# Kernel tuning notes

Measured on AMD Instinct MI355X. Metric: run time of the kernel, lower is better.

Reference implementation:

```python
import jax, jax.numpy as jnp
import numpy as np

DIM = 128
HEADS = 4
DIM_HEAD = 32
N_EMBD = HEADS * DIM_HEAD  # 128
SCALE = DIM_HEAD ** -0.5


def conv2d(x, w, b):
    # NCHW conv, 3x3, stride 1, SAME padding (= padding=1 in torch)
    out = jax.lax.conv_general_dilated(
        x, w, window_strides=(1, 1), padding='SAME',
        dimension_numbers=('NCHW', 'OIHW', 'NCHW'))
    return out + b[None, :, None, None]


def conv_block(x, w1, b1, w2, b2):
    # Conv -> ReLU -> Conv (the to_q/to_k/to_v pattern)
    return conv2d(jax.nn.relu(conv2d(x, w1, b1)), w2, b2)


def setup_inputs() -> dict:
    key = jax.random.key(0)
    ks = jax.random.split(key, 20)
    B, C, S = 4, DIM, 32
    H, W = 128, 512
    wscale = 0.05

    def cw(k, cout, cin):
        return jax.random.normal(k, (cout, cin, 3, 3), jnp.float32) * wscale

    inp = {
        'x': jax.random.normal(ks[0], (B, C, S, S), jnp.float32),
        'y': jax.random.normal(ks[1], (B, C, H, W), jnp.float32),
        'u': jax.random.randint(ks[2], (B, S, S), 0, W),
        'q_w1': cw(ks[3], N_EMBD, DIM), 'q_b1': jnp.zeros((N_EMBD,), jnp.float32),
        'q_w2': cw(ks[4], N_EMBD, N_EMBD), 'q_b2': jnp.zeros((N_EMBD,), jnp.float32),
        'k_w1': cw(ks[5], N_EMBD, DIM), 'k_b1': jnp.zeros((N_EMBD,), jnp.float32),
        'k_w2': cw(ks[6], N_EMBD, N_EMBD), 'k_b2': jnp.zeros((N_EMBD,), jnp.float32),
        'v_w1': cw(ks[7], N_EMBD, DIM), 'v_b1': jnp.zeros((N_EMBD,), jnp.float32),
        'v_w2': cw(ks[8], N_EMBD, N_EMBD), 'v_b2': jnp.zeros((N_EMBD,), jnp.float32),
        'proj_w': cw(ks[9], DIM, N_EMBD), 'proj_b': jnp.zeros((DIM,), jnp.float32),
    }
    return inp


def reference(x, y, u, q_w1, q_b1, q_w2, q_b2, k_w1, k_b1, k_w2, k_b2,
              v_w1, v_b1, v_w2, v_b2, proj_w, proj_b):
    B, C, S, _ = x.shape
    _, _, H, W = y.shape
    SS = S * S

    # Q from the (B,C,S,S) query grid -> (B, S^2, n_embd)
    q = conv_block(x, q_w1, q_b1, q_w2, q_b2).reshape(B, N_EMBD, SS).transpose(0, 2, 1)

    # K, V from the (B,C,H,W) map
    k = conv_block(y, k_w1, k_b1, k_w2, k_b2)  # (B, E, H, W)
    v = conv_block(y, v_w1, v_b1, v_w2, v_b2)

    # Gather columns of K/V along W per query index u (clamped)
    uc = jnp.clip(u, 0, W - 1).astype(jnp.int32).reshape(B, 1, 1, SS)
    ks = jnp.take_along_axis(k, uc, axis=3).transpose(0, 3, 2, 1)  # (B, SS, H, E)
    vs = jnp.take_along_axis(v, uc, axis=3).transpose(0, 3, 2, 1)  # (B, SS, H, E)

    # Per-query attention over the H axis
    dot = SCALE * jnp.einsum('bqe,bqhe->bqh', q, ks)  # (B, SS, H)
    attn = jax.nn.softmax(dot, axis=-1)
    a = jnp.einsum('bqh,bqhe->bqe', attn, vs)  # (B, SS, E)

    a = a.transpose(0, 2, 1).reshape(B, N_EMBD, S, S)
    z = jax.nn.relu(conv2d(a, proj_w, proj_b))  # (B, DIM, S, S)
    return z
```

## Files before the change

### kernel.cpp

```cpp
#include <hip/hip_runtime.h>
#include <stdint.h>

typedef __attribute__((ext_vector_type(16))) float f32x16;
typedef __attribute__((ext_vector_type(8))) short s16x8;

__device__ inline short bf16b(float f) {
  uint32_t x = __float_as_uint(f);
  return (short)((x + 0x7fffu + ((x >> 16) & 1u)) >> 16);
}
__device__ inline float bfu(uint16_t u) { return __uint_as_float(((uint32_t)u) << 16); }

__device__ inline void gll16(const void* g, void* l) {
  __builtin_amdgcn_global_load_lds((const __attribute__((address_space(1))) void*)g,
                                   (__attribute__((address_space(3))) void*)l, 16, 0, 0);
}

__global__ __launch_bounds__(256) void packw_k(
    const float* w0, const float* w1, const float* w2, const float* w3,
    const float* w4, const float* w5, const float* w6, s16x8* dst) {
  const float* srcs[7] = {w0, w1, w2, w3, w4, w5, w6};
  const int widx = blockIdx.y;
  const float* src = srcs[widx];
  const int gid = blockIdx.x * 256 + threadIdx.x;
  const int lane = gid & 63, frag = gid >> 6;
  const int nblk = frag & 3, ks = (frag >> 2) & 1, chunk = (frag >> 3) & 3, tap = frag >> 5;
  const int co = nblk * 32 + (lane & 31);
  const int cib = chunk * 32 + ks * 16 + (lane >> 5) * 8;
  s16x8 v;
#pragma unroll
  for (int j = 0; j < 8; ++j)
    v[j] = bf16b(src[((size_t)co * 128 + cib + j) * 9 + tap]);
  dst[(size_t)widx * 18432 + (size_t)frag * 64 + lane] = v;
}

template <int TW>
__global__ __launch_bounds__(256) void nchw2nhwc_k(
    const float* __restrict__ in, uint16_t* __restrict__ out, int H, int W) {
  __shared__ float tile[128][TW + 1];
  const int b = blockIdx.z, h = blockIdx.y, w0 = blockIdx.x * TW;
  for (int idx = threadIdx.x; idx < 128 * TW; idx += 256) {
    int c = idx / TW, w = idx - c * TW;
    tile[c][w] = in[(((size_t)b * 128 + c) * H + h) * W + w0 + w];
  }
  __syncthreads();
  for (int idx = threadIdx.x; idx < TW * 16; idx += 256) {
    int w = idx >> 4, cg = idx & 15;
    s16x8 v;
#pragma unroll
    for (int j = 0; j < 8; ++j) v[j] = bf16b(tile[cg * 8 + j][w]);
    *reinterpret_cast<s16x8*>(out + ((((size_t)b * H + h) * W + w0 + w) << 7) + cg * 8) = v;
  }
}

template <int OMODE, bool RELU, typename Tout>
__global__ __launch_bounds__(256, 3) void convmf4_k(
    const uint16_t* __restrict__ in, const s16x8* __restrict__ wpk,
    const float* __restrict__ bias, Tout* __restrict__ out,
    const uint16_t* __restrict__ zp, int H, int W) {
  constexpr int CP = 34, RP = 6, RPCP = RP * CP;
  constexpr int SLOTS = 4 * RPCP;
  constexpr int SPT = 4;
  __shared__ s16x8 lds[2][SPT * 256];
  const int b = blockIdx.z, r0 = blockIdx.y * 4, c0 = blockIdx.x * 32;
  const int tid = threadIdx.x, lane = tid & 63, wn = tid >> 6;
  const int wbase = tid & 192;

  const uint16_t* gsrc[SPT];
#pragma unroll
  for (int i = 0; i < SPT; ++i) {
    const int s = tid + i * 256;
    const int kq = s / RPCP;
    const int rem = s - kq * RPCP;
    const int r = rem / CP, c = rem - r * CP;
    const int gr = r0 + r - 1, gc = c0 + c - 1;
    const bool ok = (s < SLOTS) && gr >= 0 && gr < H && gc >= 0 && gc < W;
    gsrc[i] = ok ? (in + (((size_t)b * H + gr) * W + gc) * 128 + kq * 8) : zp;
  }

  const s16x8* __restrict__ wbl = wpk + wn * 64 + lane;
  s16x8 wf[9];
#pragma unroll
  for (int t = 0; t < 9; ++t) wf[t] = wbl[t * 2048];

#pragma unroll
  for (int i = 0; i < SPT; ++i) gll16(gsrc[i], &lds[0][wbase + i * 256]);

  f32x16 acc[4];
#pragma unroll
  for (int i = 0; i < 4; ++i)
#pragma unroll
    for (int r = 0; r < 16; ++r) acc[i][r] = 0.f;

  const int abase = (lane >> 5) * RPCP + (lane & 31);
  __syncthreads();

#pragma unroll
  for (int chunk = 0; chunk < 4; ++chunk) {
    const int cb = chunk & 1;
    if (chunk < 3) {
#pragma unroll
      for (int i = 0; i < SPT; ++i)
        gll16(gsrc[i] + (chunk + 1) * 32, &lds[cb ^ 1][wbase + i * 256]);
    }
    const s16x8* __restrict__ Lb = &lds[cb][abase];
#pragma unroll
    for (int ks = 0; ks < 2; ++ks) {
#pragma unroll
      for (int kx = 0; kx < 3; ++kx) {
        s16x8 ar[6];
#pragma unroll
        for (int r = 0; r < 6; ++r) ar[r] = Lb[ks * 2 * RPCP + r * CP + kx];
        __builtin_amdgcn_s_setprio(1);
#pragma unroll
        for (int ky = 0; ky < 3; ++ky) {
#pragma unroll
          for (int mf = 0; mf < 4; ++mf)
            acc[mf] = __builtin_amdgcn_mfma_f32_32x32x16_bf16(ar[mf + ky], wf[ky * 3 + kx],
                                                              acc[mf], 0, 0, 0);
        }
        __builtin_amdgcn_s_setprio(0);
        if (!(chunk == 3 && ks == 1)) {
          const int nc = (ks == 0) ? chunk : chunk + 1;
          const int nks = (ks == 0) ? 1 : 0;
#pragma unroll
          for (int ky = 0; ky < 3; ++ky) {
            const int tap = ky * 3 + kx;
            wf[tap] = wbl[((tap * 4 + nc) * 2 + nks) * 256];
          }
        }
      }
    }
    if (chunk < 3) __syncthreads();
  }

  const int co = wn * 32 + (lane & 31);
  const float bv = bias[co];
#pragma unroll
  for (int mf = 0; mf < 4; ++mf) {
    const int gr = r0 + mf;
#pragma unroll
    for (int reg = 0; reg < 16; ++reg) {
      const int gc = c0 + (reg & 3) + 8 * (reg >> 2) + 4 * (lane >> 5);
      float v = acc[mf][reg] + bv;
      if (RELU) v = fmaxf(v, 0.f);
      size_t idx;
      if (OMODE == 0)      idx = (((size_t)b * H + gr) * W + gc) * 128 + co;
      else if (OMODE == 1) idx = (((size_t)b * W + gc) * H + gr) * 128 + co;
      else                 idx = (((size_t)b * 128 + co) * H + gr) * W + gc;
      if constexpr (sizeof(Tout) == 2) ((uint16_t*)out)[idx] = (uint16_t)bf16b(v);
      else out[idx] = v;
    }
  }
}

__global__ __launch_bounds__(128) void attn_dot_k(
    const float* __restrict__ qg, const uint16_t* __restrict__ Kg,
    const int* __restrict__ u, float* __restrict__ pout) {
  const int bs = blockIdx.x;
  const int b = bs >> 10;
  const int tid = threadIdx.x;
  __shared__ float sq[128], sd[128];
  sq[tid] = qg[(size_t)bs * 128 + tid];
  int w = u[bs]; w = w < 0 ? 0 : (w > 511 ? 511 : w);
  __syncthreads();
  const uint32_t* kp = reinterpret_cast<const uint32_t*>(
      Kg + (((size_t)b * 512 + w) * 128 + tid) * 128);
  float acc = 0.f;
#pragma unroll 8
  for (int i = 0; i < 64; ++i) {
    uint32_t v = kp[i];
    acc = fmaf(sq[2 * i],     __uint_as_float(v << 16), acc);
    acc = fmaf(sq[2 * i + 1], __uint_as_float(v & 0xffff0000u), acc);
  }
  sd[tid] = acc * 0.17677669529663687f;
  __syncthreads();
  float mx = -1e30f;
  for (int i = 0; i < 128; ++i) mx = fmaxf(mx, sd[i]);
  float e = expf(sd[tid] - mx);
  __syncthreads();
  sd[tid] = e;
  __syncthreads();
  float sum = 0.f;
  for (int i = 0; i < 128; ++i) sum += sd[i];
  pout[(size_t)bs * 128 + tid] = e / sum;
}

__global__ __launch_bounds__(128) void attn_pv_k(
    const float* __restrict__ pin, const uint16_t* __restrict__ Vg,
    const int* __restrict__ u, uint16_t* __restrict__ aout) {
  const int bs = blockIdx.x;
  const int b = bs >> 10;
  const int tid = threadIdx.x;
  __shared__ float sp[128];
  sp[tid] = pin[(size_t)bs * 128 + tid];
  int w = u[bs]; w = w < 0 ? 0 : (w > 511 ? 511 : w);
  __syncthreads();
  const uint16_t* vp = Vg + ((size_t)b * 512 + w) * 16384 + tid;
  float acc = 0.f;
#pragma unroll 8
  for (int h = 0; h < 128; ++h)
    acc = fmaf(sp[h], bfu(vp[h * 128]), acc);
  aout[(size_t)bs * 128 + tid] = (uint16_t)bf16b(acc);
}

extern "C" void kernel_launch(void* const* d_in, const int* in_sizes, int n_in,
                              void* d_out, int out_size, void* d_ws, size_t ws_size,
                              hipStream_t stream) {
  const float* x      = (const float*)d_in[0];
  const float* y      = (const float*)d_in[1];
  const int*   u      = (const int*)d_in[2];
  const float* q_w1   = (const float*)d_in[3];
  const float* q_b1   = (const float*)d_in[4];
  const float* q_w2   = (const float*)d_in[5];
  const float* q_b2   = (const float*)d_in[6];
  const float* k_w1   = (const float*)d_in[7];
  const float* k_b1   = (const float*)d_in[8];
  const float* k_w2   = (const float*)d_in[9];
  const float* k_b2   = (const float*)d_in[10];
  const float* v_w1   = (const float*)d_in[11];
  const float* v_b1   = (const float*)d_in[12];
  const float* v_w2   = (const float*)d_in[13];
  const float* v_b2   = (const float*)d_in[14];
  const float* proj_w = (const float*)d_in[15];
  const float* proj_b = (const float*)d_in[16];
  float* out = (float*)d_out;

  char* ws = (char*)d_ws;
  const size_t MB = 1 << 20;
  const size_t BIG = 64 * MB;
  const bool tierB = ws_size >= 203 * MB;
  uint16_t* A  = (uint16_t*)ws;
  uint16_t* Bb = (uint16_t*)(ws + BIG);
  uint16_t* KV = tierB ? (uint16_t*)(ws + 2 * BIG) : A;
  char* sm = ws + (tierB ? 3 : 2) * BIG;
  float*    qg  = (float*)sm;
  float*    pb  = (float*)(sm + 2 * MB);
  uint16_t* xbf = (uint16_t*)(sm + 4 * MB);
  uint16_t* t1  = (uint16_t*)(sm + 5 * MB);
  uint16_t* ab  = (uint16_t*)(sm + 6 * MB);
  s16x8*    wpk = (s16x8*)(sm + 7 * MB);
  uint16_t* zp  = (uint16_t*)(sm + 10 * MB);

  hipMemsetAsync(zp, 0, 1024, stream);
  packw_k<<<dim3(72, 7), 256, 0, stream>>>(q_w1, q_w2, k_w1, k_w2, v_w1, v_w2, proj_w, wpk);
  nchw2nhwc_k<32><<<dim3(1, 32, 4), 256, 0, stream>>>(x, xbf, 32, 32);
  nchw2nhwc_k<64><<<dim3(8, 128, 4), 256, 0, stream>>>(y, A, 128, 512);
  convmf4_k<0, true,  uint16_t><<<dim3(1, 8, 4), 256, 0, stream>>>(xbf, wpk + 0 * 18432, q_b1, t1, zp, 32, 32);
  convmf4_k<0, false, float   ><<<dim3(1, 8, 4), 256, 0, stream>>>(t1,  wpk + 1 * 18432, q_b2, qg, zp, 32, 32);
  convmf4_k<0, true,  uint16_t><<<dim3(16, 32, 4), 256, 0, stream>>>(A,  wpk + 2 * 18432, k_b1, Bb, zp, 128, 512);
  convmf4_k<1, false, uint16_t><<<dim3(16, 32, 4), 256, 0, stream>>>(Bb, wpk + 3 * 18432, k_b2, KV, zp, 128, 512);
  attn_dot_k<<<dim3(4096), 128, 0, stream>>>(qg, KV, u, pb);
  if (!tierB) nchw2nhwc_k<64><<<dim3(8, 128, 4), 256, 0, stream>>>(y, A, 128, 512);
  convmf4_k<0, true,  uint16_t><<<dim3(16, 32, 4), 256, 0, stream>>>(A,  wpk + 4 * 18432, v_b1, Bb, zp, 128, 512);
  convmf4_k<1, false, uint16_t><<<dim3(16, 32, 4), 256, 0, stream>>>(Bb, wpk + 5 * 18432, v_b2, KV, zp, 128, 512);
  attn_pv_k<<<dim3(4096), 128, 0, stream>>>(pb, KV, u, ab);
  convmf4_k<3, true, float><<<dim3(1, 8, 4), 256, 0, stream>>>(ab, wpk + 6 * 18432, proj_b, out, zp, 32, 32);
}
```

Measured before the change: 438.0 us.

## Triple-buffer conv input tiles with explicit vmcnt waits and raw barriers

Changes the implicit-GEMM conv kernel from double to triple buffering of LDS input chunks. Two chunks are prefetched up front, and each later prefetch is issued after compute, so global loads run two chunks ahead. Full __syncthreads are replaced with s_waitcnt vmcnt counts plus raw s_barrier, so only the needed loads are waited on. This costs more LDS per block, which may reduce occupancy, and the hand-tuned vmcnt counts depend on how many weight loads are still outstanding.

New measurement: 433.4 us. Within noise of the previous version (-1.0%).

```diff
diff --git a/kernel.cpp b/kernel.cpp
--- a/kernel.cpp
+++ b/kernel.cpp
@@ -3,6 +3,8 @@
 
 typedef __attribute__((ext_vector_type(16))) float f32x16;
 typedef __attribute__((ext_vector_type(8))) short s16x8;
+
+#define WAITVM(n) asm volatile("s_waitcnt vmcnt(" #n ")" ::: "memory")
 
 __device__ inline short bf16b(float f) {
   uint32_t x = __float_as_uint(f);
@@ -53,14 +55,14 @@
 }
 
 template <int OMODE, bool RELU, typename Tout>
-__global__ __launch_bounds__(256, 3) void convmf4_k(
+__global__ __launch_bounds__(256, 3) void convmf5_k(
     const uint16_t* __restrict__ in, const s16x8* __restrict__ wpk,
     const float* __restrict__ bias, Tout* __restrict__ out,
     const uint16_t* __restrict__ zp, int H, int W) {
   constexpr int CP = 34, RP = 6, RPCP = RP * CP;
   constexpr int SLOTS = 4 * RPCP;
   constexpr int SPT = 4;
-  __shared__ s16x8 lds[2][SPT * 256];
+  __shared__ s16x8 lds[3][SPT * 256];
   const int b = blockIdx.z, r0 = blockIdx.y * 4, c0 = blockIdx.x * 32;
   const int tid = threadIdx.x, lane = tid & 63, wn = tid >> 6;
   const int wbase = tid & 192;
@@ -84,6 +86,8 @@
 
 #pragma unroll
   for (int i = 0; i < SPT; ++i) gll16(gsrc[i], &lds[0][wbase + i * 256]);
+#pragma unroll
+  for (int i = 0; i < SPT; ++i) gll16(gsrc[i] + 32, &lds[1][wbase + i * 256]);
 
   f32x16 acc[4];
 #pragma unroll
@@ -92,17 +96,13 @@
     for (int r = 0; r < 16; ++r) acc[i][r] = 0.f;
 
   const int abase = (lane >> 5) * RPCP + (lane & 31);
-  __syncthreads();
+  WAITVM(6);
+  __builtin_amdgcn_s_barrier();
+  __builtin_amdgcn_sched_barrier(0);
 
 #pragma unroll
   for (int chunk = 0; chunk < 4; ++chunk) {
-    const int cb = chunk & 1;
-    if (chunk < 3) {
-#pragma unroll
-      for (int i = 0; i < SPT; ++i)
-        gll16(gsrc[i] + (chunk + 1) * 32, &lds[cb ^ 1][wbase + i * 256]);
-    }
-    const s16x8* __restrict__ Lb = &lds[cb][abase];
+    const s16x8* __restrict__ Lb = &lds[chunk % 3][abase];
 #pragma unroll
     for (int ks = 0; ks < 2; ++ks) {
 #pragma unroll
@@ -130,7 +130,21 @@
         }
       }
     }
-    if (chunk < 3) __syncthreads();
+    __builtin_amdgcn_sched_barrier(0);
+    if (chunk < 2) {
+#pragma unroll
+      for (int i = 0; i < SPT; ++i)
+        gll16(gsrc[i] + (chunk + 2) * 32, &lds[(chunk + 2) % 3][wbase + i * 256]);
+    }
+    if (chunk == 0 || chunk == 1) {
+      WAITVM(24);
+      __builtin_amdgcn_s_barrier();
+      __builtin_amdgcn_sched_barrier(0);
+    } else if (chunk == 2) {
+      WAITVM(18);
+      __builtin_amdgcn_s_barrier();
+      __builtin_amdgcn_sched_barrier(0);
+    }
   }
 
   const int co = wn * 32 + (lane & 31);
@@ -245,14 +259,14 @@
   packw_k<<<dim3(72, 7), 256, 0, stream>>>(q_w1, q_w2, k_w1, k_w2, v_w1, v_w2, proj_w, wpk);
   nchw2nhwc_k<32><<<dim3(1, 32, 4), 256, 0, stream>>>(x, xbf, 32, 32);
   nchw2nhwc_k<64><<<dim3(8, 128, 4), 256, 0, stream>>>(y, A, 128, 512);
-  convmf4_k<0, true,  uint16_t><<<dim3(1, 8, 4), 256, 0, stream>>>(xbf, wpk + 0 * 18432, q_b1, t1, zp, 32, 32);
-  convmf4_k<0, false, float   ><<<dim3(1, 8, 4), 256, 0, stream>>>(t1,  wpk + 1 * 18432, q_b2, qg, zp, 32, 32);
-  convmf4_k<0, true,  uint16_t><<<dim3(16, 32, 4), 256, 0, stream>>>(A,  wpk + 2 * 18432, k_b1, Bb, zp, 128, 512);
-  convmf4_k<1, false, uint16_t><<<dim3(16, 32, 4), 256, 0, stream>>>(Bb, wpk + 3 * 18432, k_b2, KV, zp, 128, 512);
+  convmf5_k<0, true,  uint16_t><<<dim3(1, 8, 4), 256, 0, stream>>>(xbf, wpk + 0 * 18432, q_b1, t1, zp, 32, 32);
+  convmf5_k<0, false, float   ><<<dim3(1, 8, 4), 256, 0, stream>>>(t1,  wpk + 1 * 18432, q_b2, qg, zp, 32, 32);
+  convmf5_k<0, true,  uint16_t><<<dim3(16, 32, 4), 256, 0, stream>>>(A,  wpk + 2 * 18432, k_b1, Bb, zp, 128, 512);
+  convmf5_k<1, false, uint16_t><<<dim3(16, 32, 4), 256, 0, stream>>>(Bb, wpk + 3 * 18432, k_b2, KV, zp, 128, 512);
   attn_dot_k<<<dim3(4096), 128, 0, stream>>>(qg, KV, u, pb);
   if (!tierB) nchw2nhwc_k<64><<<dim3(8, 128, 4), 256, 0, stream>>>(y, A, 128, 512);
-  convmf4_k<0, true,  uint16_t><<<dim3(16, 32, 4), 256, 0, stream>>>(A,  wpk + 4 * 18432, v_b1, Bb, zp, 128, 512);
-  convmf4_k<1, false, uint16_t><<<dim3(16, 32, 4), 256, 0, stream>>>(Bb, wpk + 5 * 18432, v_b2, KV, zp, 128, 512);
+  convmf5_k<0, true,  uint16_t><<<dim3(16, 32, 4), 256, 0, stream>>>(A,  wpk + 4 * 18432, v_b1, Bb, zp, 128, 512);
+  convmf5_k<1, false, uint16_t><<<dim3(16, 32, 4), 256, 0, stream>>>(Bb, wpk + 5 * 18432, v_b2, KV, zp, 128, 512);
   attn_pv_k<<<dim3(4096), 128, 0, stream>>>(pb, KV, u, ab);
-  convmf4_k<3, true, float><<<dim3(1, 8, 4), 256, 0, stream>>>(ab, wpk + 6 * 18432, proj_b, out, zp, 32, 32);
-}
+  convmf5_k<3, true, float><<<dim3(1, 8, 4), 256, 0, stream>>>(ab, wpk + 6 * 18432, proj_b, out, zp, 32, 32);
+}
```

## Enlarge conv tile to 8 rows with 2x2 wave layout for halo reuse

Applied to the files above, without the earlier changes.

The implicit-GEMM conv kernel now processes 8 output rows per block instead of 4. Its four waves are arranged 2x2 over rows and output channels, and each wave computes two 32-channel fragments. The halo overhead of the loaded input tile drops (10 rows loaded for 8 outputs instead of 6 for 4), and each activation fragment read from LDS feeds twice as many MFMAs. In exchange, accumulator registers double and occupancy is lowered to 2 blocks per SM, and the small 32x32 convs get fewer blocks.

Result: slower. 506.4 us (+15.6%).

```diff
diff --git a/kernel.cpp b/kernel.cpp
--- a/kernel.cpp
+++ b/kernel.cpp
@@ -53,16 +53,17 @@
 }
 
 template <int OMODE, bool RELU, typename Tout>
-__global__ __launch_bounds__(256, 3) void convmf4_k(
+__global__ __launch_bounds__(256, 2) void convmf6_k(
     const uint16_t* __restrict__ in, const s16x8* __restrict__ wpk,
     const float* __restrict__ bias, Tout* __restrict__ out,
     const uint16_t* __restrict__ zp, int H, int W) {
-  constexpr int CP = 34, RP = 6, RPCP = RP * CP;
+  constexpr int CP = 34, RP = 10, RPCP = RP * CP;
   constexpr int SLOTS = 4 * RPCP;
-  constexpr int SPT = 4;
+  constexpr int SPT = 6;
   __shared__ s16x8 lds[2][SPT * 256];
-  const int b = blockIdx.z, r0 = blockIdx.y * 4, c0 = blockIdx.x * 32;
-  const int tid = threadIdx.x, lane = tid & 63, wn = tid >> 6;
+  const int b = blockIdx.z, r0 = blockIdx.y * 8, c0 = blockIdx.x * 32;
+  const int tid = threadIdx.x, lane = tid & 63;
+  const int wv = tid >> 6, wm = wv >> 1, wn = wv & 1;
   const int wbase = tid & 192;
 
   const uint16_t* gsrc[SPT];
@@ -77,21 +78,26 @@
     gsrc[i] = ok ? (in + (((size_t)b * H + gr) * W + gc) * 128 + kq * 8) : zp;
   }
 
-  const s16x8* __restrict__ wbl = wpk + wn * 64 + lane;
-  s16x8 wf[9];
-#pragma unroll
-  for (int t = 0; t < 9; ++t) wf[t] = wbl[t * 2048];
+  const s16x8* __restrict__ wbl = wpk + wn * 128 + lane;
+  s16x8 wf[9][2];
+#pragma unroll
+  for (int t = 0; t < 9; ++t) {
+    wf[t][0] = wbl[t * 2048];
+    wf[t][1] = wbl[t * 2048 + 64];
+  }
 
 #pragma unroll
   for (int i = 0; i < SPT; ++i) gll16(gsrc[i], &lds[0][wbase + i * 256]);
 
-  f32x16 acc[4];
+  f32x16 acc[4][2];
 #pragma unroll
   for (int i = 0; i < 4; ++i)
 #pragma unroll
-    for (int r = 0; r < 16; ++r) acc[i][r] = 0.f;
-
-  const int abase = (lane >> 5) * RPCP + (lane & 31);
+    for (int j = 0; j < 2; ++j)
+#pragma unroll
+      for (int r = 0; r < 16; ++r) acc[i][j][r] = 0.f;
+
+  const int abase = wm * 4 * CP + (lane >> 5) * RPCP + (lane & 31);
   __syncthreads();
 
 #pragma unroll
@@ -113,10 +119,14 @@
         __builtin_amdgcn_s_setprio(1);
 #pragma unroll
         for (int ky = 0; ky < 3; ++ky) {
-#pragma unroll
-          for (int mf = 0; mf < 4; ++mf)
-            acc[mf] = __builtin_amdgcn_mfma_f32_32x32x16_bf16(ar[mf + ky], wf[ky * 3 + kx],
-                                                              acc[mf], 0, 0, 0);
+          const int tap = ky * 3 + kx;
+#pragma unroll
+          for (int mf = 0; mf < 4; ++mf) {
+            acc[mf][0] = __builtin_amdgcn_mfma_f32_32x32x16_bf16(ar[mf + ky], wf[tap][0],
+                                                                 acc[mf][0], 0, 0, 0);
+            acc[mf][1] = __builtin_amdgcn_mfma_f32_32x32x16_bf16(ar[mf + ky], wf[tap][1],
+                                                                 acc[mf][1], 0, 0, 0);
+          }
         }
         __builtin_amdgcn_s_setprio(0);
         if (!(chunk == 3 && ks == 1)) {
@@ -125,7 +135,9 @@
 #pragma unroll
           for (int ky = 0; ky < 3; ++ky) {
             const int tap = ky * 3 + kx;
-            wf[tap] = wbl[((tap * 4 + nc) * 2 + nks) * 256];
+            const int off = ((tap * 4 + nc) * 2 + nks) * 256;
+            wf[tap][0] = wbl[off];
+            wf[tap][1] = wbl[off + 64];
           }
         }
       }
@@ -133,22 +145,25 @@
     if (chunk < 3) __syncthreads();
   }
 
-  const int co = wn * 32 + (lane & 31);
-  const float bv = bias[co];
-#pragma unroll
-  for (int mf = 0; mf < 4; ++mf) {
-    const int gr = r0 + mf;
-#pragma unroll
-    for (int reg = 0; reg < 16; ++reg) {
-      const int gc = c0 + (reg & 3) + 8 * (reg >> 2) + 4 * (lane >> 5);
-      float v = acc[mf][reg] + bv;
-      if (RELU) v = fmaxf(v, 0.f);
-      size_t idx;
-      if (OMODE == 0)      idx = (((size_t)b * H + gr) * W + gc) * 128 + co;
-      else if (OMODE == 1) idx = (((size_t)b * W + gc) * H + gr) * 128 + co;
-      else                 idx = (((size_t)b * 128 + co) * H + gr) * W + gc;
-      if constexpr (sizeof(Tout) == 2) ((uint16_t*)out)[idx] = (uint16_t)bf16b(v);
-      else out[idx] = v;
+#pragma unroll
+  for (int nf = 0; nf < 2; ++nf) {
+    const int co = wn * 64 + nf * 32 + (lane & 31);
+    const float bv = bias[co];
+#pragma unroll
+    for (int mf = 0; mf < 4; ++mf) {
+      const int gr = r0 + wm * 4 + mf;
+#pragma unroll
+      for (int reg = 0; reg < 16; ++reg) {
+        const int gc = c0 + (reg & 3) + 8 * (reg >> 2) + 4 * (lane >> 5);
+        float v = acc[mf][nf][reg] + bv;
+        if (RELU) v = fmaxf(v, 0.f);
+        size_t idx;
+        if (OMODE == 0)      idx = (((size_t)b * H + gr) * W + gc) * 128 + co;
+        else if (OMODE == 1) idx = (((size_t)b * W + gc) * H + gr) * 128 + co;
+        else                 idx = (((size_t)b * 128 + co) * H + gr) * W + gc;
+        if constexpr (sizeof(Tout) == 2) ((uint16_t*)out)[idx] = (uint16_t)bf16b(v);
+        else out[idx] = v;
+      }
     }
   }
 }
@@ -245,14 +260,14 @@
   packw_k<<<dim3(72, 7), 256, 0, stream>>>(q_w1, q_w2, k_w1, k_w2, v_w1, v_w2, proj_w, wpk);
   nchw2nhwc_k<32><<<dim3(1, 32, 4), 256, 0, stream>>>(x, xbf, 32, 32);
   nchw2nhwc_k<64><<<dim3(8, 128, 4), 256, 0, stream>>>(y, A, 128, 512);
-  convmf4_k<0, true,  uint16_t><<<dim3(1, 8, 4), 256, 0, stream>>>(xbf, wpk + 0 * 18432, q_b1, t1, zp, 32, 32);
-  convmf4_k<0, false, float   ><<<dim3(1, 8, 4), 256, 0, stream>>>(t1,  wpk + 1 * 18432, q_b2, qg, zp, 32, 32);
-  convmf4_k<0, true,  uint16_t><<<dim3(16, 32, 4), 256, 0, stream>>>(A,  wpk + 2 * 18432, k_b1, Bb, zp, 128, 512);
-  convmf4_k<1, false, uint16_t><<<dim3(16, 32, 4), 256, 0, stream>>>(Bb, wpk + 3 * 18432, k_b2, KV, zp, 128, 512);
+  convmf6_k<0, true,  uint16_t><<<dim3(1, 4, 4), 256, 0, stream>>>(xbf, wpk + 0 * 18432, q_b1, t1, zp, 32, 32);
+  convmf6_k<0, false, float   ><<<dim3(1, 4, 4), 256, 0, stream>>>(t1,  wpk + 1 * 18432, q_b2, qg, zp, 32, 32);
+  convmf6_k<0, true,  uint16_t><<<dim3(16, 16, 4), 256, 0, stream>>>(A,  wpk + 2 * 18432, k_b1, Bb, zp, 128, 512);
+  convmf6_k<1, false, uint16_t><<<dim3(16, 16, 4), 256, 0, stream>>>(Bb, wpk + 3 * 18432, k_b2, KV, zp, 128, 512);
   attn_dot_k<<<dim3(4096), 128, 0, stream>>>(qg, KV, u, pb);
   if (!tierB) nchw2nhwc_k<64><<<dim3(8, 128, 4), 256, 0, stream>>>(y, A, 128, 512);
-  convmf4_k<0, true,  uint16_t><<<dim3(16, 32, 4), 256, 0, stream>>>(A,  wpk + 4 * 18432, v_b1, Bb, zp, 128, 512);
-  convmf4_k<1, false, uint16_t><<<dim3(16, 32, 4), 256, 0, stream>>>(Bb, wpk + 5 * 18432, v_b2, KV, zp, 128, 512);
+  convmf6_k<0, true,  uint16_t><<<dim3(16, 16, 4), 256, 0, stream>>>(A,  wpk + 4 * 18432, v_b1, Bb, zp, 128, 512);
+  convmf6_k<1, false, uint16_t><<<dim3(16, 16, 4), 256, 0, stream>>>(Bb, wpk + 5 * 18432, v_b2, KV, zp, 128, 512);
   attn_pv_k<<<dim3(4096), 128, 0, stream>>>(pb, KV, u, ab);
-  convmf4_k<3, true, float><<<dim3(1, 8, 4), 256, 0, stream>>>(ab, wpk + 6 * 18432, proj_b, out, zp, 32, 32);
-}
+  convmf6_k<3, true, float><<<dim3(1, 4, 4), 256, 0, stream>>>(ab, wpk + 6 * 18432, proj_b, out, zp, 32, 32);
+}
```

## Interleave async LDS prefetch with MFMA phases using explicit barriers and waitcnts

Applied to the files above, without the earlier changes.

Restructures the conv kernel's main loop into six phases per chunk. Each phase issues one of the next-chunk global-to-LDS loads after reading its A fragments, then runs the MFMAs between explicit s_barrier, lgkmcnt and vmcnt waits, replacing the per-chunk __syncthreads. The goal is to spread the prefetch traffic across the compute and avoid a full drain at chunk boundaries. In exchange it adds more barriers per chunk and relies on hand-tuned waitcnt values such as vmcnt(9), which must match the number of outstanding loads to stay correct.

Result: no change. 434.5 us (-0.8%).

```diff
diff --git a/kernel.cpp b/kernel.cpp
--- a/kernel.cpp
+++ b/kernel.cpp
@@ -3,6 +3,9 @@
 
 typedef __attribute__((ext_vector_type(16))) float f32x16;
 typedef __attribute__((ext_vector_type(8))) short s16x8;
+
+#define WAITVM(n) asm volatile("s_waitcnt vmcnt(" #n ")" ::: "memory")
+#define WAITLGKM0 asm volatile("s_waitcnt lgkmcnt(0)" ::: "memory")
 
 __device__ inline short bf16b(float f) {
   uint32_t x = __float_as_uint(f);
@@ -53,7 +56,7 @@
 }
 
 template <int OMODE, bool RELU, typename Tout>
-__global__ __launch_bounds__(256, 3) void convmf4_k(
+__global__ __launch_bounds__(256, 3) void convmf7_k(
     const uint16_t* __restrict__ in, const s16x8* __restrict__ wpk,
     const float* __restrict__ bias, Tout* __restrict__ out,
     const uint16_t* __restrict__ zp, int H, int W) {
@@ -92,45 +95,48 @@
     for (int r = 0; r < 16; ++r) acc[i][r] = 0.f;
 
   const int abase = (lane >> 5) * RPCP + (lane & 31);
-  __syncthreads();
+  WAITVM(0);
+  __builtin_amdgcn_s_barrier();
+  __builtin_amdgcn_sched_barrier(0);
 
 #pragma unroll
   for (int chunk = 0; chunk < 4; ++chunk) {
     const int cb = chunk & 1;
-    if (chunk < 3) {
-#pragma unroll
-      for (int i = 0; i < SPT; ++i)
-        gll16(gsrc[i] + (chunk + 1) * 32, &lds[cb ^ 1][wbase + i * 256]);
-    }
     const s16x8* __restrict__ Lb = &lds[cb][abase];
 #pragma unroll
-    for (int ks = 0; ks < 2; ++ks) {
-#pragma unroll
-      for (int kx = 0; kx < 3; ++kx) {
-        s16x8 ar[6];
-#pragma unroll
-        for (int r = 0; r < 6; ++r) ar[r] = Lb[ks * 2 * RPCP + r * CP + kx];
-        __builtin_amdgcn_s_setprio(1);
+    for (int p = 0; p < 6; ++p) {
+      const int ks = p / 3, kx = p - ks * 3;
+      s16x8 ar[6];
+#pragma unroll
+      for (int r = 0; r < 6; ++r) ar[r] = Lb[ks * 2 * RPCP + r * CP + kx];
+      if (chunk < 3 && p < SPT)
+        gll16(gsrc[p] + (chunk + 1) * 32, &lds[cb ^ 1][wbase + p * 256]);
+      __builtin_amdgcn_sched_barrier(0);
+      __builtin_amdgcn_s_barrier();
+      WAITLGKM0;
+      __builtin_amdgcn_sched_barrier(0);
+      __builtin_amdgcn_s_setprio(1);
+#pragma unroll
+      for (int ky = 0; ky < 3; ++ky) {
+#pragma unroll
+        for (int mf = 0; mf < 4; ++mf)
+          acc[mf] = __builtin_amdgcn_mfma_f32_32x32x16_bf16(ar[mf + ky], wf[ky * 3 + kx],
+                                                            acc[mf], 0, 0, 0);
+      }
+      __builtin_amdgcn_s_setprio(0);
+      if (!(chunk == 3 && ks == 1)) {
+        const int nc = (ks == 0) ? chunk : chunk + 1;
+        const int nks = (ks == 0) ? 1 : 0;
 #pragma unroll
         for (int ky = 0; ky < 3; ++ky) {
-#pragma unroll
-          for (int mf = 0; mf < 4; ++mf)
-            acc[mf] = __builtin_amdgcn_mfma_f32_32x32x16_bf16(ar[mf + ky], wf[ky * 3 + kx],
-                                                              acc[mf], 0, 0, 0);
-        }
-        __builtin_amdgcn_s_setprio(0);
-        if (!(chunk == 3 && ks == 1)) {
-          const int nc = (ks == 0) ? chunk : chunk + 1;
-          const int nks = (ks == 0) ? 1 : 0;
-#pragma unroll
-          for (int ky = 0; ky < 3; ++ky) {
-            const int tap = ky * 3 + kx;
-            wf[tap] = wbl[((tap * 4 + nc) * 2 + nks) * 256];
-          }
+          const int tap = ky * 3 + kx;
+          wf[tap] = wbl[((tap * 4 + nc) * 2 + nks) * 256];
         }
       }
+      __builtin_amdgcn_sched_barrier(0);
+      if (p == 5 && chunk < 3) WAITVM(9);
+      __builtin_amdgcn_s_barrier();
     }
-    if (chunk < 3) __syncthreads();
   }
 
   const int co = wn * 32 + (lane & 31);
@@ -245,14 +251,14 @@
   packw_k<<<dim3(72, 7), 256, 0, stream>>>(q_w1, q_w2, k_w1, k_w2, v_w1, v_w2, proj_w, wpk);
   nchw2nhwc_k<32><<<dim3(1, 32, 4), 256, 0, stream>>>(x, xbf, 32, 32);
   nchw2nhwc_k<64><<<dim3(8, 128, 4), 256, 0, stream>>>(y, A, 128, 512);
-  convmf4_k<0, true,  uint16_t><<<dim3(1, 8, 4), 256, 0, stream>>>(xbf, wpk + 0 * 18432, q_b1, t1, zp, 32, 32);
-  convmf4_k<0, false, float   ><<<dim3(1, 8, 4), 256, 0, stream>>>(t1,  wpk + 1 * 18432, q_b2, qg, zp, 32, 32);
-  convmf4_k<0, true,  uint16_t><<<dim3(16, 32, 4), 256, 0, stream>>>(A,  wpk + 2 * 18432, k_b1, Bb, zp, 128, 512);
-  convmf4_k<1, false, uint16_t><<<dim3(16, 32, 4), 256, 0, stream>>>(Bb, wpk + 3 * 18432, k_b2, KV, zp, 128, 512);
+  convmf7_k<0, true,  uint16_t><<<dim3(1, 8, 4), 256, 0, stream>>>(xbf, wpk + 0 * 18432, q_b1, t1, zp, 32, 32);
+  convmf7_k<0, false, float   ><<<dim3(1, 8, 4), 256, 0, stream>>>(t1,  wpk + 1 * 18432, q_b2, qg, zp, 32, 32);
+  convmf7_k<0, true,  uint16_t><<<dim3(16, 32, 4), 256, 0, stream>>>(A,  wpk + 2 * 18432, k_b1, Bb, zp, 128, 512);
+  convmf7_k<1, false, uint16_t><<<dim3(16, 32, 4), 256, 0, stream>>>(Bb, wpk + 3 * 18432, k_b2, KV, zp, 128, 512);
   attn_dot_k<<<dim3(4096), 128, 0, stream>>>(qg, KV, u, pb);
   if (!tierB) nchw2nhwc_k<64><<<dim3(8, 128, 4), 256, 0, stream>>>(y, A, 128, 512);
-  convmf4_k<0, true,  uint16_t><<<dim3(16, 32, 4), 256, 0, stream>>>(A,  wpk + 4 * 18432, v_b1, Bb, zp, 128, 512);
-  convmf4_k<1, false, uint16_t><<<dim3(16, 32, 4), 256, 0, stream>>>(Bb, wpk + 5 * 18432, v_b2, KV, zp, 128, 512);
+  convmf7_k<0, true,  uint16_t><<<dim3(16, 32, 4), 256, 0, stream>>>(A,  wpk + 4 * 18432, v_b1, Bb, zp, 128, 512);
+  convmf7_k<1, false, uint16_t><<<dim3(16, 32, 4), 256, 0, stream>>>(Bb, wpk + 5 * 18432, v_b2, KV, zp, 128, 512);
   attn_pv_k<<<dim3(4096), 128, 0, stream>>>(pb, KV, u, ab);
-  convmf4_k<3, true, float><<<dim3(1, 8, 4), 256, 0, stream>>>(ab, wpk + 6 * 18432, proj_b, out, zp, 32, 32);
-}
+  convmf7_k<3, true, float><<<dim3(1, 8, 4), 256, 0, stream>>>(ab, wpk + 6 * 18432, proj_b, out, zp, 32, 32);
+}
```
